# Performance work log

Measured on AMD Instinct MI355X. Metric: run time of the kernel, lower is better.

Reference implementation:

```python
import jax, jax.numpy as jnp
import numpy as np

D_MODEL = 768
NUM_HEADS = 12
D_K = D_MODEL // NUM_HEADS


def setup_inputs() -> dict:
    key = jax.random.key(0)
    ks = jax.random.split(key, 11)
    B, L = 1, 4096
    s = 1.0 / np.sqrt(D_MODEL)
    return {
        "q": jax.random.normal(ks[0], (B, L, D_MODEL), jnp.float32),
        "k": jax.random.normal(ks[1], (B, L, D_MODEL), jnp.float32),
        "v": jax.random.normal(ks[2], (B, L, D_MODEL), jnp.float32),
        "Wq": jax.random.normal(ks[3], (D_MODEL, D_MODEL), jnp.float32) * s,
        "bq": jax.random.normal(ks[4], (D_MODEL,), jnp.float32) * s,
        "Wk": jax.random.normal(ks[5], (D_MODEL, D_MODEL), jnp.float32) * s,
        "bk": jax.random.normal(ks[6], (D_MODEL,), jnp.float32) * s,
        "Wv": jax.random.normal(ks[7], (D_MODEL, D_MODEL), jnp.float32) * s,
        "bv": jax.random.normal(ks[8], (D_MODEL,), jnp.float32) * s,
        "Wo": jax.random.normal(ks[9], (D_MODEL, D_MODEL), jnp.float32) * s,
        "bo": jax.random.normal(ks[10], (D_MODEL,), jnp.float32) * s,
    }


def reference(q, k, v, Wq, bq, Wk, bk, Wv, bv, Wo, bo):
    B, L, _ = q.shape
    # linear projections (torch Linear: x @ W.T + b)
    qp = q @ Wq.T + bq
    kp = k @ Wk.T + bk
    vp = v @ Wv.T + bv
    # split heads: (B, H, L, d_k)
    def split(x):
        return x.reshape(B, L, NUM_HEADS, D_K).transpose(0, 2, 1, 3)
    qh, kh, vh = split(qp), split(kp), split(vp)
    scale = 1.0 / jnp.sqrt(jnp.asarray(D_K, qh.dtype))
    scores = jnp.einsum("bhqd,bhkd->bhqk", qh, kh) * scale  # (B,H,L,L)
    weights = jax.nn.softmax(scores, axis=-1)
    out = jnp.einsum("bhqk,bhkd->bhqd", weights, vh)
    out = out.transpose(0, 2, 1, 3).reshape(B, L, D_MODEL)
    return out @ Wo.T + bo
```

## Files before the change

### kernel.cpp

```cpp
#include <hip/hip_runtime.h>
#include <stdint.h>
#include <math.h>

#define L_SEQ  4096
#define DMODEL 768
#define NHEADS 12
#define DKH    64
#define QSCALE 0.18033688011112042f

typedef _Float16 f16;
typedef __attribute__((ext_vector_type(8))) _Float16 half8;
typedef __attribute__((ext_vector_type(4))) _Float16 half4;
typedef __attribute__((ext_vector_type(4))) float f32x4;
typedef __attribute__((ext_vector_type(4))) float fv4;
typedef __attribute__((ext_vector_type(16))) float f32x16;
typedef __attribute__((ext_vector_type(4))) unsigned int uint4v;

#define MFMA16(a, b, c) __builtin_amdgcn_mfma_f32_16x16x32_f16(a, b, c, 0, 0, 0)
#define MFMA32(a, b, c) __builtin_amdgcn_mfma_f32_32x32x16_f16(a, b, c, 0, 0, 0)

#define NE ((size_t)L_SEQ * DMODEL)
#define WE ((size_t)DMODEL * DMODEL)

static __device__ __forceinline__ unsigned int pack2(float a, float b) {
  return __builtin_bit_cast(unsigned int, __builtin_amdgcn_cvt_pkrtz(a, b));
}

__global__ __launch_bounds__(256)
void cvt_w(const float* __restrict__ Wq, const float* __restrict__ Wk,
           const float* __restrict__ Wv, const float* __restrict__ Wo,
           f16* __restrict__ w16)
{
  const size_t WE4 = WE / 4;
  size_t i = (size_t)blockIdx.x * 256 + threadIdx.x;
  const float* srcs[4] = {Wq, Wk, Wv, Wo};
  int r = (int)(i / WE4);
  size_t off = i - (size_t)r * WE4;
  float4 f = reinterpret_cast<const float4*>(srcs[r])[off];
  half4 h; h[0] = (f16)f.x; h[1] = (f16)f.y; h[2] = (f16)f.z; h[3] = (f16)f.w;
  reinterpret_cast<half4*>(w16 + (size_t)r * WE)[off] = h;
}

__global__ __launch_bounds__(256)
void qkv_gemm(const float* __restrict__ xq, const float* __restrict__ xk,
              const float* __restrict__ xv, const f16* __restrict__ w16,
              const float* __restrict__ bq, const float* __restrict__ bk,
              const float* __restrict__ bv,
              f16* __restrict__ Qp, f16* __restrict__ Kp, f16* __restrict__ VpT)
{
  __shared__ f16 As[128][72];
  __shared__ f16 Bs[128][72];
  const int tid  = threadIdx.x;
  const int lane = tid & 63, wid = tid >> 6;
  const int lq   = lane & 15, quad = lane >> 4;
  const int wm   = (wid & 1) * 64, wn = (wid >> 1) * 64;

  const int d   = blockIdx.x;
  const int r8  = d & 7;
  const int j   = d >> 3;
  const int g   = r8 + 8 * (j / 6);
  const int nb  = j % 6;
  const int widx = g / 32;
  const int m0   = (g % 32) * 128;
  const int n0   = nb * 128;

  const float* X = (widx == 0) ? xq : (widx == 1) ? xk : xv;
  const f16* W = w16 + (size_t)widx * WE;
  const float* Bv = (widx == 0) ? bq : (widx == 1) ? bk : bv;

  const int arow = tid >> 1, aseg = (tid & 1) * 32;
  const float* aptr = X + (size_t)(m0 + arow) * DMODEL + aseg;
  const f16*   bptr = W + (size_t)(n0 + arow) * DMODEL + aseg;

  fv4 a4[8];
#pragma unroll
  for (int u = 0; u < 8; ++u) a4[u] = reinterpret_cast<const fv4*>(aptr)[u];
  half8 b4[4];
#pragma unroll
  for (int u = 0; u < 4; ++u) b4[u] = reinterpret_cast<const half8*>(bptr)[u];

  f32x4 acc[4][4] = {};

  for (int k0 = 0; k0 < DMODEL; k0 += 64) {
#pragma unroll
    for (int u = 0; u < 4; ++u) {
      half8 h;
#pragma unroll
      for (int e = 0; e < 4; ++e) {
        h[e]     = (f16)a4[2 * u][e];
        h[4 + e] = (f16)a4[2 * u + 1][e];
      }
      *reinterpret_cast<half8*>(&As[arow][aseg + u * 8]) = h;
      *reinterpret_cast<half8*>(&Bs[arow][aseg + u * 8]) = b4[u];
    }
    __syncthreads();

    if (k0 + 64 < DMODEL) {
#pragma unroll
      for (int u = 0; u < 8; ++u)
        a4[u] = reinterpret_cast<const fv4*>(aptr + k0 + 64)[u];
#pragma unroll
      for (int u = 0; u < 4; ++u)
        b4[u] = reinterpret_cast<const half8*>(bptr + k0 + 64)[u];
    }

#pragma unroll
    for (int ks = 0; ks < 2; ++ks) {
      half8 bf[4];
#pragma unroll
      for (int nf = 0; nf < 4; ++nf)
        bf[nf] = *reinterpret_cast<half8*>(&Bs[wn + nf * 16 + lq][ks * 32 + quad * 8]);
#pragma unroll
      for (int mf = 0; mf < 4; ++mf) {
        half8 af = *reinterpret_cast<half8*>(&As[wm + mf * 16 + lq][ks * 32 + quad * 8]);
#pragma unroll
        for (int nf = 0; nf < 4; ++nf)
          acc[mf][nf] = MFMA16(af, bf[nf], acc[mf][nf]);
      }
    }
    __syncthreads();
  }

#pragma unroll
  for (int nf = 0; nf < 4; ++nf) {
    const int col  = n0 + wn + nf * 16 + lq;
    const float bias = Bv[col];
#pragma unroll
    for (int mf = 0; mf < 4; ++mf) {
      const int rowb = m0 + wm + mf * 16 + quad * 4;
      if (widx == 2) {
        half4 o4;
#pragma unroll
        for (int r = 0; r < 4; ++r) o4[r] = (f16)(acc[mf][nf][r] + bias);
        *reinterpret_cast<half4*>(VpT + (size_t)col * L_SEQ + rowb) = o4;
      } else if (widx == 0) {
#pragma unroll
        for (int r = 0; r < 4; ++r)
          Qp[(size_t)(rowb + r) * DMODEL + col] = (f16)((acc[mf][nf][r] + bias) * QSCALE);
      } else {
#pragma unroll
        for (int r = 0; r < 4; ++r)
          Kp[(size_t)(rowb + r) * DMODEL + col] = (f16)(acc[mf][nf][r] + bias);
      }
    }
  }
}

__global__ __launch_bounds__(256, 3)
void attn_mfma4(const f16* __restrict__ Qp, const f16* __restrict__ Kp,
                const f16* __restrict__ VpT, f16* __restrict__ AO)
{
  const int h  = blockIdx.x;
  const int q0 = blockIdx.y * 64;
  const int tid  = threadIdx.x;
  const int lane = tid & 63, wid = tid >> 6;
  const int l31  = lane & 31, hc = lane >> 5;
  const int qh   = wid & 1, kh = wid >> 1;

  __shared__ __align__(16) char smem[36864];
  f16 (*Ks)[64][72] = (f16 (*)[64][72])smem;
  f16 (*Vt)[64][72] = (f16 (*)[64][72])(smem + 18432);
  float* Of  = (float*)smem;
  float* lf  = (float*)(smem + 16384);
  f16*   Of16 = (f16*)(smem + 16640);

  half8 qf[4];
#pragma unroll
  for (int st = 0; st < 4; ++st)
    qf[st] = *reinterpret_cast<const half8*>(
        Qp + (size_t)(q0 + qh * 32 + l31) * DMODEL + h * DKH + st * 16 + hc * 8);

  f32x16 oacc[2] = {};
  float lsum = 0.0f;

  const int srow = tid >> 2, sseg = (tid & 3) * 16;
  const f16* kbase = Kp  + (size_t)srow * DMODEL + h * DKH + sseg;
  const f16* vbase = VpT + (size_t)(h * DKH + srow) * L_SEQ + sseg;

  half8 k0 = *reinterpret_cast<const half8*>(kbase);
  half8 k1 = *reinterpret_cast<const half8*>(kbase + 8);
  half8 v0 = *reinterpret_cast<const half8*>(vbase);
  half8 v1 = *reinterpret_cast<const half8*>(vbase + 8);

  int p = 0;
  for (int kt = 0; kt < L_SEQ; kt += 64) {
    *reinterpret_cast<half8*>(&Ks[p][srow][sseg])     = k0;
    *reinterpret_cast<half8*>(&Ks[p][srow][sseg + 8]) = k1;
    *reinterpret_cast<half8*>(&Vt[p][srow][sseg])     = v0;
    *reinterpret_cast<half8*>(&Vt[p][srow][sseg + 8]) = v1;
    __syncthreads();

    if (kt + 64 < L_SEQ) {
      const f16* kn = kbase + (size_t)(kt + 64) * DMODEL;
      const f16* vn = vbase + (kt + 64);
      k0 = *reinterpret_cast<const half8*>(kn);
      k1 = *reinterpret_cast<const half8*>(kn + 8);
      v0 = *reinterpret_cast<const half8*>(vn);
      v1 = *reinterpret_cast<const half8*>(vn + 8);
    }

    __builtin_amdgcn_s_setprio(1);

    f32x16 s = {};
#pragma unroll
    for (int st = 0; st < 4; ++st) {
      half8 kf = *reinterpret_cast<half8*>(&Ks[p][kh * 32 + l31][st * 16 + hc * 8]);
      s = MFMA32(kf, qf[st], s);
    }

    unsigned int pk[8];
#pragma unroll
    for (int i = 0; i < 8; ++i) {
      float p0 = __builtin_amdgcn_exp2f(s[2 * i]);
      float p1 = __builtin_amdgcn_exp2f(s[2 * i + 1]);
      lsum += p0 + p1;
      pk[i] = pack2(p0, p1);
    }

#pragma unroll
    for (int st = 0; st < 2; ++st) {
      unsigned int w0 = pk[4 * st + 0], w1 = pk[4 * st + 1];
      unsigned int w2 = pk[4 * st + 2], w3 = pk[4 * st + 3];
      asm("v_permlane32_swap_b32 %0, %1" : "+v"(w0), "+v"(w2));
      asm("v_permlane32_swap_b32 %0, %1" : "+v"(w1), "+v"(w3));
      uint4v pw; pw[0] = w0; pw[1] = w1; pw[2] = w2; pw[3] = w3;
      half8 pf = __builtin_bit_cast(half8, pw);
#pragma unroll
      for (int a = 0; a < 2; ++a) {
        half8 vf = *reinterpret_cast<half8*>(&Vt[p][a * 32 + l31][kh * 32 + st * 16 + hc * 8]);
        oacc[a] = MFMA32(vf, pf, oacc[a]);
      }
    }
    __builtin_amdgcn_s_setprio(0);
    p ^= 1;
  }
  __syncthreads();

  float lw = lsum + __shfl_xor(lsum, 32);

  if (kh == 0) {
#pragma unroll
    for (int a = 0; a < 2; ++a)
#pragma unroll
      for (int r = 0; r < 16; ++r) {
        int d = a * 32 + (r & 3) + 8 * (r >> 2) + 4 * hc;
        Of[((qh * 64) + d) * 32 + l31] = oacc[a][r];
      }
    if (lane < 32) lf[qh * 32 + l31] = lw;
  }
  __syncthreads();
  if (kh == 1) {
    const float inv = 1.0f / (lf[qh * 32 + l31] + lw);
#pragma unroll
    for (int a = 0; a < 2; ++a)
#pragma unroll
      for (int r = 0; r < 16; ++r) {
        int d = a * 32 + (r & 3) + 8 * (r >> 2) + 4 * hc;
        float val = (Of[((qh * 64) + d) * 32 + l31] + oacc[a][r]) * inv;
        Of16[(qh * 32 + l31) * 64 + d] = (f16)val;
      }
  }
  __syncthreads();

  *reinterpret_cast<half8*>(AO + (size_t)(q0 + srow) * DMODEL + h * DKH + sseg) =
      *reinterpret_cast<half8*>(&Of16[srow * 64 + sseg]);
  *reinterpret_cast<half8*>(AO + (size_t)(q0 + srow) * DMODEL + h * DKH + sseg + 8) =
      *reinterpret_cast<half8*>(&Of16[srow * 64 + sseg + 8]);
}

__global__ __launch_bounds__(256)
void out_gemm(const f16* __restrict__ A, const f16* __restrict__ W,
              const float* __restrict__ Bv, float* __restrict__ O)
{
  __shared__ f16 As[64][72];
  __shared__ f16 Bs[64][72];
  const int tid  = threadIdx.x;
  const int lane = tid & 63, wid = tid >> 6;
  const int lq   = lane & 15, quad = lane >> 4;
  const int wm   = (wid & 1) * 32, wn = (wid >> 1) * 32;

  const int d   = blockIdx.x;
  const int r8  = d & 7;
  const int j   = d >> 3;
  const int g   = r8 + 8 * (j / 12);
  const int nb  = j % 12;
  const int m0  = g * 64, n0 = nb * 64;

  const int row = tid >> 2, seg = (tid & 3) * 16;
  const f16* aptr = A + (size_t)(m0 + row) * DMODEL + seg;
  const f16* bptr = W + (size_t)(n0 + row) * DMODEL + seg;

  half8 a0 = *reinterpret_cast<const half8*>(aptr);
  half8 a1 = *reinterpret_cast<const half8*>(aptr + 8);
  half8 b0 = *reinterpret_cast<const half8*>(bptr);
  half8 b1 = *reinterpret_cast<const half8*>(bptr + 8);

  f32x4 acc[2][2] = {};

  for (int k0 = 0; k0 < DMODEL; k0 += 64) {
    *reinterpret_cast<half8*>(&As[row][seg])     = a0;
    *reinterpret_cast<half8*>(&As[row][seg + 8]) = a1;
    *reinterpret_cast<half8*>(&Bs[row][seg])     = b0;
    *reinterpret_cast<half8*>(&Bs[row][seg + 8]) = b1;
    __syncthreads();

    if (k0 + 64 < DMODEL) {
      a0 = *reinterpret_cast<const half8*>(aptr + k0 + 64);
      a1 = *reinterpret_cast<const half8*>(aptr + k0 + 72);
      b0 = *reinterpret_cast<const half8*>(bptr + k0 + 64);
      b1 = *reinterpret_cast<const half8*>(bptr + k0 + 72);
    }

#pragma unroll
    for (int ks = 0; ks < 2; ++ks) {
      half8 bf[2];
#pragma unroll
      for (int nf = 0; nf < 2; ++nf)
        bf[nf] = *reinterpret_cast<half8*>(&Bs[wn + nf * 16 + lq][ks * 32 + quad * 8]);
#pragma unroll
      for (int mf = 0; mf < 2; ++mf) {
        half8 af = *reinterpret_cast<half8*>(&As[wm + mf * 16 + lq][ks * 32 + quad * 8]);
#pragma unroll
        for (int nf = 0; nf < 2; ++nf)
          acc[mf][nf] = MFMA16(af, bf[nf], acc[mf][nf]);
      }
    }
    __syncthreads();
  }

#pragma unroll
  for (int nf = 0; nf < 2; ++nf) {
    const int col = n0 + wn + nf * 16 + lq;
    const float bias = Bv[col];
#pragma unroll
    for (int mf = 0; mf < 2; ++mf) {
      const int rowb = m0 + wm + mf * 16 + quad * 4;
#pragma unroll
      for (int r = 0; r < 4; ++r)
        O[(size_t)(rowb + r) * DMODEL + col] = acc[mf][nf][r] + bias;
    }
  }
}

extern "C" void kernel_launch(void* const* d_in, const int* in_sizes, int n_in,
                              void* d_out, int out_size, void* d_ws, size_t ws_size,
                              hipStream_t stream) {
  const float* q  = (const float*)d_in[0];
  const float* k  = (const float*)d_in[1];
  const float* v  = (const float*)d_in[2];
  const float* Wq = (const float*)d_in[3];
  const float* bq = (const float*)d_in[4];
  const float* Wk = (const float*)d_in[5];
  const float* bk = (const float*)d_in[6];
  const float* Wv = (const float*)d_in[7];
  const float* bv = (const float*)d_in[8];
  const float* Wo = (const float*)d_in[9];
  const float* bo = (const float*)d_in[10];
  float* out = (float*)d_out;

  f16* w16 = (f16*)d_ws;
  f16* Qp  = w16 + 4 * WE;
  f16* Kp  = Qp + NE;
  f16* VpT = Kp + NE;
  f16* AO  = VpT + NE;

  const int ncvt = (int)(WE / 256);
  cvt_w<<<ncvt, 256, 0, stream>>>(Wq, Wk, Wv, Wo, w16);

  qkv_gemm<<<576, 256, 0, stream>>>(q, k, v, w16, bq, bk, bv, Qp, Kp, VpT);

  dim3 gattn(NHEADS, L_SEQ / 64);
  attn_mfma4<<<gattn, 256, 0, stream>>>(Qp, Kp, VpT, AO);

  out_gemm<<<768, 256, 0, stream>>>(AO, w16 + 3 * WE, bo, out);
}
```

Before: 231.9 us.

## Pre-convert activations to fp16 and enlarge output GEMM tiles to 128x128

Merges weight and activation fp32-to-fp16 conversion into one pre-pass kernel so the QKV GEMM loads fp16 inputs without in-loop conversion. Also retiles the output projection GEMM from 64x64 to 128x128 blocks with a 4x4 MFMA fragment per wave, cutting the grid from 768 to 192 blocks. The pre-pass adds an extra full read and write of the activations. The larger tiles may leave CUs idle.

```diff
diff --git a/kernel.cpp b/kernel.cpp
--- a/kernel.cpp
+++ b/kernel.cpp
@@ -12,7 +12,6 @@
 typedef __attribute__((ext_vector_type(8))) _Float16 half8;
 typedef __attribute__((ext_vector_type(4))) _Float16 half4;
 typedef __attribute__((ext_vector_type(4))) float f32x4;
-typedef __attribute__((ext_vector_type(4))) float fv4;
 typedef __attribute__((ext_vector_type(16))) float f32x16;
 typedef __attribute__((ext_vector_type(4))) unsigned int uint4v;
 
@@ -27,23 +26,27 @@
 }
 
 __global__ __launch_bounds__(256)
-void cvt_w(const float* __restrict__ Wq, const float* __restrict__ Wk,
-           const float* __restrict__ Wv, const float* __restrict__ Wo,
-           f16* __restrict__ w16)
+void cvt_all(const float* __restrict__ q, const float* __restrict__ k,
+             const float* __restrict__ v, const float* __restrict__ Wq,
+             const float* __restrict__ Wk, const float* __restrict__ Wv,
+             const float* __restrict__ Wo, f16* __restrict__ x16,
+             f16* __restrict__ w16)
 {
-  const size_t WE4 = WE / 4;
+  const size_t NE4 = NE / 4, WE4 = WE / 4;
   size_t i = (size_t)blockIdx.x * 256 + threadIdx.x;
-  const float* srcs[4] = {Wq, Wk, Wv, Wo};
-  int r = (int)(i / WE4);
-  size_t off = i - (size_t)r * WE4;
+  const float* srcs[7] = {q, k, v, Wq, Wk, Wv, Wo};
+  f16* dsts[7] = {x16, x16 + NE, x16 + 2 * NE,
+                  w16, w16 + WE, w16 + 2 * WE, w16 + 3 * WE};
+  const size_t sz4[7] = {NE4, NE4, NE4, WE4, WE4, WE4, WE4};
+  int r = 0; size_t off = i;
+  while (off >= sz4[r]) { off -= sz4[r]; ++r; }
   float4 f = reinterpret_cast<const float4*>(srcs[r])[off];
   half4 h; h[0] = (f16)f.x; h[1] = (f16)f.y; h[2] = (f16)f.z; h[3] = (f16)f.w;
-  reinterpret_cast<half4*>(w16 + (size_t)r * WE)[off] = h;
+  reinterpret_cast<half4*>(dsts[r])[off] = h;
 }
 
 __global__ __launch_bounds__(256)
-void qkv_gemm(const float* __restrict__ xq, const float* __restrict__ xk,
-              const float* __restrict__ xv, const f16* __restrict__ w16,
+void qkv_gemm(const f16* __restrict__ x16, const f16* __restrict__ w16,
               const float* __restrict__ bq, const float* __restrict__ bk,
               const float* __restrict__ bv,
               f16* __restrict__ Qp, f16* __restrict__ Kp, f16* __restrict__ VpT)
@@ -64,44 +67,37 @@
   const int m0   = (g % 32) * 128;
   const int n0   = nb * 128;
 
-  const float* X = (widx == 0) ? xq : (widx == 1) ? xk : xv;
+  const f16* X = x16 + (size_t)widx * NE;
   const f16* W = w16 + (size_t)widx * WE;
   const float* Bv = (widx == 0) ? bq : (widx == 1) ? bk : bv;
 
-  const int arow = tid >> 1, aseg = (tid & 1) * 32;
-  const float* aptr = X + (size_t)(m0 + arow) * DMODEL + aseg;
-  const f16*   bptr = W + (size_t)(n0 + arow) * DMODEL + aseg;
-
-  fv4 a4[8];
-#pragma unroll
-  for (int u = 0; u < 8; ++u) a4[u] = reinterpret_cast<const fv4*>(aptr)[u];
-  half8 b4[4];
-#pragma unroll
-  for (int u = 0; u < 4; ++u) b4[u] = reinterpret_cast<const half8*>(bptr)[u];
+  const int srow = tid >> 1, sseg = (tid & 1) * 32;
+  const f16* aptr = X + (size_t)(m0 + srow) * DMODEL + sseg;
+  const f16* bptr = W + (size_t)(n0 + srow) * DMODEL + sseg;
+
+  half8 a4[4], b4[4];
+#pragma unroll
+  for (int u = 0; u < 4; ++u) {
+    a4[u] = reinterpret_cast<const half8*>(aptr)[u];
+    b4[u] = reinterpret_cast<const half8*>(bptr)[u];
+  }
 
   f32x4 acc[4][4] = {};
 
   for (int k0 = 0; k0 < DMODEL; k0 += 64) {
 #pragma unroll
     for (int u = 0; u < 4; ++u) {
-      half8 h;
-#pragma unroll
-      for (int e = 0; e < 4; ++e) {
-        h[e]     = (f16)a4[2 * u][e];
-        h[4 + e] = (f16)a4[2 * u + 1][e];
-      }
-      *reinterpret_cast<half8*>(&As[arow][aseg + u * 8]) = h;
-      *reinterpret_cast<half8*>(&Bs[arow][aseg + u * 8]) = b4[u];
+      *reinterpret_cast<half8*>(&As[srow][sseg + u * 8]) = a4[u];
+      *reinterpret_cast<half8*>(&Bs[srow][sseg + u * 8]) = b4[u];
     }
     __syncthreads();
 
     if (k0 + 64 < DMODEL) {
 #pragma unroll
-      for (int u = 0; u < 8; ++u)
-        a4[u] = reinterpret_cast<const fv4*>(aptr + k0 + 64)[u];
-#pragma unroll
-      for (int u = 0; u < 4; ++u)
+      for (int u = 0; u < 4; ++u) {
+        a4[u] = reinterpret_cast<const half8*>(aptr + k0 + 64)[u];
         b4[u] = reinterpret_cast<const half8*>(bptr + k0 + 64)[u];
+      }
     }
 
 #pragma unroll
@@ -272,56 +268,60 @@
 void out_gemm(const f16* __restrict__ A, const f16* __restrict__ W,
               const float* __restrict__ Bv, float* __restrict__ O)
 {
-  __shared__ f16 As[64][72];
-  __shared__ f16 Bs[64][72];
+  __shared__ f16 As[128][72];
+  __shared__ f16 Bs[128][72];
   const int tid  = threadIdx.x;
   const int lane = tid & 63, wid = tid >> 6;
   const int lq   = lane & 15, quad = lane >> 4;
-  const int wm   = (wid & 1) * 32, wn = (wid >> 1) * 32;
+  const int wm   = (wid & 1) * 64, wn = (wid >> 1) * 64;
 
   const int d   = blockIdx.x;
   const int r8  = d & 7;
   const int j   = d >> 3;
-  const int g   = r8 + 8 * (j / 12);
-  const int nb  = j % 12;
-  const int m0  = g * 64, n0 = nb * 64;
-
-  const int row = tid >> 2, seg = (tid & 3) * 16;
-  const f16* aptr = A + (size_t)(m0 + row) * DMODEL + seg;
-  const f16* bptr = W + (size_t)(n0 + row) * DMODEL + seg;
-
-  half8 a0 = *reinterpret_cast<const half8*>(aptr);
-  half8 a1 = *reinterpret_cast<const half8*>(aptr + 8);
-  half8 b0 = *reinterpret_cast<const half8*>(bptr);
-  half8 b1 = *reinterpret_cast<const half8*>(bptr + 8);
-
-  f32x4 acc[2][2] = {};
+  const int g   = r8 + 8 * (j / 6);
+  const int nb  = j % 6;
+  const int m0  = g * 128, n0 = nb * 128;
+
+  const int srow = tid >> 1, sseg = (tid & 1) * 32;
+  const f16* aptr = A + (size_t)(m0 + srow) * DMODEL + sseg;
+  const f16* bptr = W + (size_t)(n0 + srow) * DMODEL + sseg;
+
+  half8 a4[4], b4[4];
+#pragma unroll
+  for (int u = 0; u < 4; ++u) {
+    a4[u] = reinterpret_cast<const half8*>(aptr)[u];
+    b4[u] = reinterpret_cast<const half8*>(bptr)[u];
+  }
+
+  f32x4 acc[4][4] = {};
 
   for (int k0 = 0; k0 < DMODEL; k0 += 64) {
-    *reinterpret_cast<half8*>(&As[row][seg])     = a0;
-    *reinterpret_cast<half8*>(&As[row][seg + 8]) = a1;
-    *reinterpret_cast<half8*>(&Bs[row][seg])     = b0;
-    *reinterpret_cast<half8*>(&Bs[row][seg + 8]) = b1;
+#pragma unroll
+    for (int u = 0; u < 4; ++u) {
+      *reinterpret_cast<half8*>(&As[srow][sseg + u * 8]) = a4[u];
+      *reinterpret_cast<half8*>(&Bs[srow][sseg + u * 8]) = b4[u];
+    }
     __syncthreads();
 
     if (k0 + 64 < DMODEL) {
-      a0 = *reinterpret_cast<const half8*>(aptr + k0 + 64);
-      a1 = *reinterpret_cast<const half8*>(aptr + k0 + 72);
-      b0 = *reinterpret_cast<const half8*>(bptr + k0 + 64);
-      b1 = *reinterpret_cast<const half8*>(bptr + k0 + 72);
+#pragma unroll
+      for (int u = 0; u < 4; ++u) {
+        a4[u] = reinterpret_cast<const half8*>(aptr + k0 + 64)[u];
+        b4[u] = reinterpret_cast<const half8*>(bptr + k0 + 64)[u];
+      }
     }
 
 #pragma unroll
     for (int ks = 0; ks < 2; ++ks) {
-      half8 bf[2];
-#pragma unroll
-      for (int nf = 0; nf < 2; ++nf)
+      half8 bf[4];
+#pragma unroll
+      for (int nf = 0; nf < 4; ++nf)
         bf[nf] = *reinterpret_cast<half8*>(&Bs[wn + nf * 16 + lq][ks * 32 + quad * 8]);
 #pragma unroll
-      for (int mf = 0; mf < 2; ++mf) {
+      for (int mf = 0; mf < 4; ++mf) {
         half8 af = *reinterpret_cast<half8*>(&As[wm + mf * 16 + lq][ks * 32 + quad * 8]);
 #pragma unroll
-        for (int nf = 0; nf < 2; ++nf)
+        for (int nf = 0; nf < 4; ++nf)
           acc[mf][nf] = MFMA16(af, bf[nf], acc[mf][nf]);
       }
     }
@@ -329,11 +329,11 @@
   }
 
 #pragma unroll
-  for (int nf = 0; nf < 2; ++nf) {
+  for (int nf = 0; nf < 4; ++nf) {
     const int col = n0 + wn + nf * 16 + lq;
     const float bias = Bv[col];
 #pragma unroll
-    for (int mf = 0; mf < 2; ++mf) {
+    for (int mf = 0; mf < 4; ++mf) {
       const int rowb = m0 + wm + mf * 16 + quad * 4;
 #pragma unroll
       for (int r = 0; r < 4; ++r)
@@ -358,19 +358,20 @@
   const float* bo = (const float*)d_in[10];
   float* out = (float*)d_out;
 
-  f16* w16 = (f16*)d_ws;
+  f16* x16 = (f16*)d_ws;
+  f16* w16 = x16 + 3 * NE;
   f16* Qp  = w16 + 4 * WE;
   f16* Kp  = Qp + NE;
   f16* VpT = Kp + NE;
   f16* AO  = VpT + NE;
 
-  const int ncvt = (int)(WE / 256);
-  cvt_w<<<ncvt, 256, 0, stream>>>(Wq, Wk, Wv, Wo, w16);
-
-  qkv_gemm<<<576, 256, 0, stream>>>(q, k, v, w16, bq, bk, bv, Qp, Kp, VpT);
+  const int ncvt = (int)((3 * (NE / 4) + 4 * (WE / 4)) / 256);
+  cvt_all<<<ncvt, 256, 0, stream>>>(q, k, v, Wq, Wk, Wv, Wo, x16, w16);
+
+  qkv_gemm<<<576, 256, 0, stream>>>(x16, w16, bq, bk, bv, Qp, Kp, VpT);
 
   dim3 gattn(NHEADS, L_SEQ / 64);
   attn_mfma4<<<gattn, 256, 0, stream>>>(Qp, Kp, VpT, AO);
 
-  out_gemm<<<768, 256, 0, stream>>>(AO, w16 + 3 * WE, bo, out);
-}
+  out_gemm<<<192, 256, 0, stream>>>(AO, w16 + 3 * WE, bo, out);
+}
```

Result: faster. 224.5 us (-3.2%).
